# Performance work log

Measured on AMD Instinct MI355X. Metric: run time of the kernel, lower is better.

The kernel has to match this reference:

```python
import jax, jax.numpy as jnp
import numpy as np

N_NODES = 50000
N_EDGES = 800000
N_GRAPHS = 128
D_IN = 64
D_H = 64
D_OUT = 16
N_GIN_LAYERS = 4  # num_layers - 1
BN_EPS = 1e-5


def setup_inputs() -> dict:
    key = jax.random.key(0)
    ks = jax.random.split(key, 12)
    s = 0.05  # weight scale for numerical sanity
    x = jax.random.normal(ks[0], (N_NODES, D_IN), dtype=jnp.float32)
    w = jax.random.uniform(ks[1], (N_EDGES,), dtype=jnp.float32)
    src = jax.random.randint(ks[2], (N_EDGES,), 0, N_NODES, dtype=jnp.int32)
    dst = jax.random.randint(ks[3], (N_EDGES,), 0, N_NODES, dtype=jnp.int32)
    graph_ids = jnp.sort(jax.random.randint(ks[4], (N_NODES,), 0, N_GRAPHS, dtype=jnp.int32))
    eps = jnp.zeros((N_GIN_LAYERS,), dtype=jnp.float32)
    mlp_W1 = jax.random.normal(ks[5], (N_GIN_LAYERS, D_IN, D_H), dtype=jnp.float32) * s
    mlp_b1 = jnp.zeros((N_GIN_LAYERS, D_H), dtype=jnp.float32)
    mlp_bn_g = jnp.ones((N_GIN_LAYERS, D_H), dtype=jnp.float32)
    mlp_bn_b = jnp.zeros((N_GIN_LAYERS, D_H), dtype=jnp.float32)
    mlp_W2 = jax.random.normal(ks[6], (N_GIN_LAYERS, D_H, D_H), dtype=jnp.float32) * s
    mlp_b2 = jnp.zeros((N_GIN_LAYERS, D_H), dtype=jnp.float32)
    bn_g = jnp.ones((N_GIN_LAYERS, D_H), dtype=jnp.float32)
    bn_b = jnp.zeros((N_GIN_LAYERS, D_H), dtype=jnp.float32)
    pred_W = jax.random.normal(ks[7], (N_GIN_LAYERS + 1, D_H, D_OUT), dtype=jnp.float32) * s
    pred_b = jnp.zeros((N_GIN_LAYERS + 1, D_OUT), dtype=jnp.float32)
    return {"x": x, "w": w, "src": src, "dst": dst, "graph_ids": graph_ids,
            "eps": eps, "mlp_W1": mlp_W1, "mlp_b1": mlp_b1,
            "mlp_bn_g": mlp_bn_g, "mlp_bn_b": mlp_bn_b,
            "mlp_W2": mlp_W2, "mlp_b2": mlp_b2,
            "bn_g": bn_g, "bn_b": bn_b, "pred_W": pred_W, "pred_b": pred_b}


def _batchnorm(h, gamma, beta):
    # training-mode BatchNorm1d: normalize by batch mean / biased variance
    mu = jnp.mean(h, axis=0)
    var = jnp.mean((h - mu) ** 2, axis=0)
    return gamma * (h - mu) * jax.lax.rsqrt(var + BN_EPS) + beta


def reference(x, w, src, dst, graph_ids, eps, mlp_W1, mlp_b1, mlp_bn_g, mlp_bn_b,
              mlp_W2, mlp_b2, bn_g, bn_b, pred_W, pred_b):
    def pool(h):  # graph readout: sum over nodes of each graph -> [G, D]
        return jax.ops.segment_sum(h, graph_ids, num_segments=N_GRAPHS)

    h = x
    # layer-0 prediction on raw features (dropout p=0 -> identity)
    score = pool(h) @ pred_W[0] + pred_b[0]
    for l in range(N_GIN_LAYERS):
        # message: edge weight * source feature, reduce: sum over in-edges
        msg = w[:, None] * h[src]                                  # [E, D]
        h_neigh = jax.ops.segment_sum(msg, dst, num_segments=N_NODES)
        h = (1.0 + eps[l]) * h + h_neigh                           # eps self-aggregate
        # 2-layer MLP: Linear -> BN -> ReLU -> Linear
        t = _batchnorm(h @ mlp_W1[l] + mlp_b1[l], mlp_bn_g[l], mlp_bn_b[l])
        h = jax.nn.relu(t) @ mlp_W2[l] + mlp_b2[l]
        # outer BN + ReLU
        h = jax.nn.relu(_batchnorm(h, bn_g[l], bn_b[l]))
        score = score + pool(h) @ pred_W[l + 1] + pred_b[l + 1]
    return score
```

## Files before the change

kernel.cpp:

```cpp
#include <hip/hip_runtime.h>
#include <hip/hip_bf16.h>

#define N_NODES 50000
#define N_EDGES 800000
#define N_GRAPHS 128
#define NB2 391
#define BCAP 4096
#define EPB 4096
#define PART_BLOCKS ((N_EDGES + EPB - 1) / EPB)

typedef __attribute__((ext_vector_type(8))) short short8;
typedef __attribute__((ext_vector_type(4))) float f32x4;

union B16x8 { uint4 u; short8 s; };

__device__ __forceinline__ unsigned bf16rn(float f) {
    unsigned u = __float_as_uint(f);
    return (u + 0x7FFFu + ((u >> 16) & 1u)) >> 16;
}
__device__ __forceinline__ unsigned packbf2(float a, float b) {
    return bf16rn(a) | (bf16rn(b) << 16);
}
__device__ __forceinline__ float2 unpkbf2(unsigned v) {
    return make_float2(__uint_as_float(v << 16), __uint_as_float(v & 0xFFFF0000u));
}


__global__ __launch_bounds__(256) void setup_partition_kernel(
    const int* __restrict__ dst, const int* __restrict__ src, const float* __restrict__ w,
    int* __restrict__ cursor, int2* __restrict__ tmp, int E,
    const float* __restrict__ x, unsigned* __restrict__ xb,
    const float* __restrict__ W1, const float* __restrict__ W2,
    unsigned short* __restrict__ Wt, const int* __restrict__ gid,
    int* __restrict__ start, int n, int ngraphs) {
    __shared__ int lh[NB2];
    __shared__ int lbase[NB2];
    const int t = threadIdx.x;

    const int gtid = blockIdx.x * 256 + t;
    const int gsz = gridDim.x * 256;
    for (int i = gtid; i < n * 8; i += gsz) {
        float4 a = *(const float4*)(x + (size_t)i * 8);
        float4 b = *(const float4*)(x + (size_t)i * 8 + 4);
        uint4 o;
        o.x = packbf2(a.x, a.y);
        o.y = packbf2(a.z, a.w);
        o.z = packbf2(b.x, b.y);
        o.w = packbf2(b.z, b.w);
        *(uint4*)(xb + (size_t)i * 4) = o;
    }
    for (int i = gtid; i < 8 * 4096; i += gsz) {
        int mat = i >> 12, k = (i >> 6) & 63, nn = i & 63, l = mat >> 1;
        const float* Wsrc = (mat & 1) ? (W2 + l * 4096) : (W1 + l * 4096);
        Wt[(size_t)mat * 4096 + nn * 64 + k] = (unsigned short)bf16rn(Wsrc[k * 64 + nn]);
    }
    for (int i = gtid; i < n; i += gsz) {
        int g = gid[i];
        if (i == 0) {
            for (int q = 0; q <= g; ++q) start[q] = 0;
        } else {
            int p = gid[i - 1];
            if (p != g)
                for (int q = p + 1; q <= g; ++q) start[q] = i;
        }
        if (i == n - 1)
            for (int q = g + 1; q <= ngraphs; ++q) start[q] = n;
    }

    for (int i = t; i < NB2; i += 256) lh[i] = 0;
    __syncthreads();
    int base = blockIdx.x * EPB;
    int d[EPB / 256];
#pragma unroll
    for (int i = 0; i < EPB / 256; ++i) {
        int e = base + i * 256 + t;
        d[i] = (e < E) ? dst[e] : -1;
        if (d[i] >= 0) atomicAdd(&lh[d[i] >> 7], 1);
    }
    __syncthreads();
    for (int i = t; i < NB2; i += 256) {
        int v = lh[i];
        if (v) lbase[i] = atomicAdd(&cursor[i], v);
        lh[i] = 0;
    }
    __syncthreads();
#pragma unroll
    for (int i = 0; i < EPB / 256; ++i) {
        int e = base + i * 256 + t;
        if (d[i] >= 0) {
            int b = d[i] >> 7;
            int dl = d[i] & 127;
            int rank = atomicAdd(&lh[b], 1);
            tmp[(size_t)b * BCAP + lbase[b] + rank] =
                make_int2(src[e] | (dl << 16), __float_as_int(w[e]));
        }
    }
}


__global__ __launch_bounds__(256) void node_sort_kernel(const int2* __restrict__ tmp,
                                                        const int* __restrict__ ecnt,
                                                        int2* __restrict__ row_se,
                                                        unsigned* __restrict__ pack, int n) {
    __shared__ int hist[128];
    __shared__ int run[128];
    __shared__ int s[256];
    const int t = threadIdx.x;
    const int b = blockIdx.x;
    int cnt = ecnt[b];
    if (cnt > BCAP) cnt = BCAP;
    const int2* tb2 = tmp + (size_t)b * BCAP;
    const int gbase = b * BCAP;

    if (t < 128) hist[t] = 0;
    __syncthreads();
    for (int j = t; j < cnt; j += 256) atomicAdd(&hist[(tb2[j].x >> 16) & 127], 1);
    __syncthreads();
    int v = (t < 128) ? hist[t] : 0;
    s[t] = v;
    __syncthreads();
    for (int off = 1; off < 128; off <<= 1) {
        int u = (t >= off) ? s[t - off] : 0;
        __syncthreads();
        s[t] += u;
        __syncthreads();
    }
    if (t < 128) {
        int excl = s[t] - v;
        int node = b * 128 + t;
        if (node < n) row_se[node] = make_int2(gbase + excl, gbase + excl + v);
        run[t] = gbase + excl;
    }
    __syncthreads();
    for (int j = t; j < cnt; j += 256) {
        int2 p = tb2[j];
        int pos = atomicAdd(&run[(p.x >> 16) & 127], 1);
        pack[pos] = (unsigned)(p.x & 0xFFFF) | (bf16rn(__int_as_float(p.y)) << 16);
    }
}


__global__ __launch_bounds__(256) void agg_kernel(const unsigned* __restrict__ hb,
                                                  const unsigned* __restrict__ pack,
                                                  const int2* __restrict__ row_se,
                                                  const float* __restrict__ eps, int layer,
                                                  unsigned* __restrict__ outb, int n,
                                                  const float* __restrict__ stats,
                                                  const float* __restrict__ gamma,
                                                  const float* __restrict__ beta,
                                                  int transform, int agg_blocks,
                                                  const int* __restrict__ start,
                                                  const float* __restrict__ pW,
                                                  const float* __restrict__ pb,
                                                  float* __restrict__ score) {
    __shared__ float sc[64], sh[64];
    const int t = threadIdx.x;
    if (transform) {
        if (t < 64) {
            float inv_n = 1.0f / (float)n;
            float mean = stats[t] * inv_n;
            float var = stats[64 + t] * inv_n - mean * mean;
            float s = gamma[t] * rsqrtf(var + 1e-5f);
            sc[t] = s;
            sh[t] = beta[t] - mean * s;
        }
        __syncthreads();
    }

    if ((int)blockIdx.x >= agg_blocks) {
        __shared__ float red[16][68];
        __shared__ float pl[64];
        const int g = blockIdx.x - agg_blocks;
        const int r16 = t >> 4;
        const int qq = t & 15;
        const int k0 = qq << 2;
        int i0 = start[g], i1 = start[g + 1];
        float4 ps = make_float4(0.f, 0.f, 0.f, 0.f);
        for (int i = i0 + r16; i < i1; i += 16) {
            uint2 u = *(const uint2*)(hb + (size_t)i * 32 + qq * 2);
            float2 a = unpkbf2(u.x);
            float2 b = unpkbf2(u.y);
            if (transform) {
                a.x = fmaxf(fmaf(a.x, sc[k0 + 0], sh[k0 + 0]), 0.f);
                a.y = fmaxf(fmaf(a.y, sc[k0 + 1], sh[k0 + 1]), 0.f);
                b.x = fmaxf(fmaf(b.x, sc[k0 + 2], sh[k0 + 2]), 0.f);
                b.y = fmaxf(fmaf(b.y, sc[k0 + 3], sh[k0 + 3]), 0.f);
            }
            ps.x += a.x; ps.y += a.y; ps.z += b.x; ps.w += b.y;
        }
        red[r16][k0 + 0] = ps.x;
        red[r16][k0 + 1] = ps.y;
        red[r16][k0 + 2] = ps.z;
        red[r16][k0 + 3] = ps.w;
        __syncthreads();
        if (t < 64) {
            float s = 0.f;
#pragma unroll
            for (int r = 0; r < 16; ++r) s += red[r][t];
            pl[t] = s;
        }
        __syncthreads();
        if (t < 16) {
            float s = pb[t];
#pragma unroll 8
            for (int d = 0; d < 64; ++d) s += pl[d] * pW[d * 16 + t];
            score[g * 16 + t] = transform ? (score[g * 16 + t] + s) : s;
        }
        return;
    }

    int node = blockIdx.x * 4 + (t >> 6);
    if (node >= n) return;
    const int lane = t & 63;
    const int slot = lane >> 4;
    const int li = lane & 15;

    float4 sc4 = make_float4(1.f, 1.f, 1.f, 1.f);
    float4 sh4 = make_float4(0.f, 0.f, 0.f, 0.f);
    if (transform) {
        sc4 = *(const float4*)(sc + li * 4);
        sh4 = *(const float4*)(sh + li * 4);
    }
    float e1 = 1.0f + eps[layer];

    float4 acc = make_float4(0.f, 0.f, 0.f, 0.f);
    {
        uint2 su = *(const uint2*)(hb + (size_t)node * 32 + li * 2);
        if (slot == 0) {
            float2 a = unpkbf2(su.x), b = unpkbf2(su.y);
            if (transform) {
                a.x = fmaxf(fmaf(a.x, sc4.x, sh4.x), 0.f);
                a.y = fmaxf(fmaf(a.y, sc4.y, sh4.y), 0.f);
                b.x = fmaxf(fmaf(b.x, sc4.z, sh4.z), 0.f);
                b.y = fmaxf(fmaf(b.y, sc4.w, sh4.w), 0.f);
            }
            acc.x = e1 * a.x; acc.y = e1 * a.y; acc.z = e1 * b.x; acc.w = e1 * b.y;
        }
    }

    int2 se = row_se[node];
    int j0 = se.x, j1 = se.y;
    int j = j0;
    unsigned pk[4];
    if (j < j1) {
#pragma unroll
        for (int u = 0; u < 4; ++u) {
            int idx = j + slot + u * 4;
            pk[u] = pack[idx < j1 ? idx : j1 - 1];
        }
    }
    while (j < j1) {
        float wv[4];
        uint2 g[4];
#pragma unroll
        for (int u = 0; u < 4; ++u) {
            int jj = j + slot + u * 4;
            wv[u] = (jj < j1) ? __uint_as_float(pk[u] & 0xFFFF0000u) : 0.f;
        }
#pragma unroll
        for (int u = 0; u < 4; ++u)
            g[u] = *(const uint2*)(hb + (size_t)(pk[u] & 0xFFFFu) * 32 + li * 2);
        j += 16;
        if (j < j1) {
#pragma unroll
            for (int u = 0; u < 4; ++u) {
                int idx = j + slot + u * 4;
                pk[u] = pack[idx < j1 ? idx : j1 - 1];
            }
        }
#pragma unroll
        for (int u = 0; u < 4; ++u) {
            float2 a = unpkbf2(g[u].x), b = unpkbf2(g[u].y);
            if (transform) {
                a.x = fmaxf(fmaf(a.x, sc4.x, sh4.x), 0.f);
                a.y = fmaxf(fmaf(a.y, sc4.y, sh4.y), 0.f);
                b.x = fmaxf(fmaf(b.x, sc4.z, sh4.z), 0.f);
                b.y = fmaxf(fmaf(b.y, sc4.w, sh4.w), 0.f);
            }
            acc.x += wv[u] * a.x;
            acc.y += wv[u] * a.y;
            acc.z += wv[u] * b.x;
            acc.w += wv[u] * b.y;
        }
    }

    acc.x += __shfl_xor(acc.x, 16);
    acc.y += __shfl_xor(acc.y, 16);
    acc.z += __shfl_xor(acc.z, 16);
    acc.w += __shfl_xor(acc.w, 16);
    acc.x += __shfl_xor(acc.x, 32);
    acc.y += __shfl_xor(acc.y, 32);
    acc.z += __shfl_xor(acc.z, 32);
    acc.w += __shfl_xor(acc.w, 32);
    if (slot == 0) {
        uint2 o;
        o.x = packbf2(acc.x, acc.y);
        o.y = packbf2(acc.z, acc.w);
        *(uint2*)(outb + (size_t)node * 32 + li * 2) = o;
    }
}


#define GTILE 128

__global__ __launch_bounds__(256) void mfma_gemm(const unsigned short* __restrict__ A,
                                                 const unsigned short* __restrict__ Wt,
                                                 const float* __restrict__ bias,
                                                 unsigned short* __restrict__ out,
                                                 float* __restrict__ stats_out,
                                                 const float* __restrict__ stats_in,
                                                 const float* __restrict__ gamma,
                                                 const float* __restrict__ beta,
                                                 int n, int transform) {
    __shared__ float sc[64], sh[64];
    __shared__ unsigned short cstage[GTILE * 64];
    __shared__ float rsum[64 * 17];
    __shared__ float rsq[64 * 17];

    const int t = threadIdx.x;
    if (transform && t < 64) {
        float inv_n = 1.0f / (float)n;
        float mean = stats_in[t] * inv_n;
        float var = stats_in[64 + t] * inv_n - mean * mean;
        float s = gamma[t] * rsqrtf(var + 1e-5f);
        sc[t] = s;
        sh[t] = beta[t] - mean * s;
    }
    __syncthreads();

    const int wid = t >> 6;
    const int lane = t & 63;
    const int m = lane & 15;
    const int q = lane >> 4;
    const int rowbase = blockIdx.x * GTILE + wid * 32;

    B16x8 bf[4][2];
#pragma unroll
    for (int tc = 0; tc < 4; ++tc)
#pragma unroll
        for (int kc = 0; kc < 2; ++kc)
            bf[tc][kc].u = *(const uint4*)(Wt + (size_t)(tc * 16 + m) * 64 + kc * 32 + q * 8);

    B16x8 af[2][2];
#pragma unroll
    for (int tr = 0; tr < 2; ++tr) {
        int gr = rowbase + tr * 16 + m;
#pragma unroll
        for (int kc = 0; kc < 2; ++kc) {
            if (gr < n)
                af[tr][kc].u = *(const uint4*)(A + (size_t)gr * 64 + kc * 32 + q * 8);
            else
                af[tr][kc].u = make_uint4(0, 0, 0, 0);
        }
    }

    if (transform) {
        int k0base = q * 8;
#pragma unroll
        for (int tr = 0; tr < 2; ++tr)
#pragma unroll
            for (int kc = 0; kc < 2; ++kc) {
                int k0 = kc * 32 + k0base;
                float4 s0 = *(const float4*)(sc + k0);
                float4 s1 = *(const float4*)(sc + k0 + 4);
                float4 h0 = *(const float4*)(sh + k0);
                float4 h1 = *(const float4*)(sh + k0 + 4);
                uint4 uu = af[tr][kc].u;
                float2 p0 = unpkbf2(uu.x), p1 = unpkbf2(uu.y);
                float2 p2 = unpkbf2(uu.z), p3 = unpkbf2(uu.w);
                p0.x = fmaxf(fmaf(p0.x, s0.x, h0.x), 0.f);
                p0.y = fmaxf(fmaf(p0.y, s0.y, h0.y), 0.f);
                p1.x = fmaxf(fmaf(p1.x, s0.z, h0.z), 0.f);
                p1.y = fmaxf(fmaf(p1.y, s0.w, h0.w), 0.f);
                p2.x = fmaxf(fmaf(p2.x, s1.x, h1.x), 0.f);
                p2.y = fmaxf(fmaf(p2.y, s1.y, h1.y), 0.f);
                p3.x = fmaxf(fmaf(p3.x, s1.z, h1.z), 0.f);
                p3.y = fmaxf(fmaf(p3.y, s1.w, h1.w), 0.f);
                uu.x = packbf2(p0.x, p0.y);
                uu.y = packbf2(p1.x, p1.y);
                uu.z = packbf2(p2.x, p2.y);
                uu.w = packbf2(p3.x, p3.y);
                af[tr][kc].u = uu;
            }
    }

    f32x4 acc[2][4];
#pragma unroll
    for (int tr = 0; tr < 2; ++tr)
#pragma unroll
        for (int tc = 0; tc < 4; ++tc) {
            acc[tr][tc] = (f32x4){0.f, 0.f, 0.f, 0.f};
            acc[tr][tc] = __builtin_amdgcn_mfma_f32_16x16x32_bf16(af[tr][0].s, bf[tc][0].s,
                                                                  acc[tr][tc], 0, 0, 0);
            acc[tr][tc] = __builtin_amdgcn_mfma_f32_16x16x32_bf16(af[tr][1].s, bf[tc][1].s,
                                                                  acc[tr][tc], 0, 0, 0);
        }

    float bc[4];
#pragma unroll
    for (int tc = 0; tc < 4; ++tc) bc[tc] = bias[tc * 16 + m];

    float psum[4] = {0, 0, 0, 0}, psq[4] = {0, 0, 0, 0};
#pragma unroll
    for (int tr = 0; tr < 2; ++tr)
#pragma unroll
        for (int reg = 0; reg < 4; ++reg) {
            int rl = wid * 32 + tr * 16 + q * 4 + reg;
            int gr = blockIdx.x * GTILE + rl;
            int sw = ((rl >> 2) & 3) << 4;
            bool ok = gr < n;
#pragma unroll
            for (int tc = 0; tc < 4; ++tc) {
                float val = acc[tr][tc][reg] + bc[tc];
                int col = tc * 16 + m;
                cstage[rl * 64 + (col ^ sw)] = (unsigned short)bf16rn(ok ? val : 0.f);
                if (ok) {
                    psum[tc] += val;
                    psq[tc] += val * val;
                }
            }
        }

    int contrib = wid * 4 + q;
#pragma unroll
    for (int tc = 0; tc < 4; ++tc) {
        int c = tc * 16 + m;
        rsum[c * 17 + contrib] = psum[tc];
        rsq[c * 17 + contrib] = psq[tc];
    }
    __syncthreads();

#pragma unroll
    for (int rep = 0; rep < 4; ++rep) {
        int idx = rep * 256 + t;
        int rl = idx >> 3;
        int k = idx & 7;
        int gr = blockIdx.x * GTILE + rl;
        if (gr < n) {
            int klds = k ^ (((rl >> 2) & 3) << 1);
            uint4 v = *(const uint4*)(cstage + rl * 64 + klds * 8);
            *(uint4*)(out + (size_t)gr * 64 + k * 8) = v;
        }
    }

    if (t < 64) {
        float s = 0.f, qq = 0.f;
#pragma unroll
        for (int i = 0; i < 16; ++i) {
            s += rsum[t * 17 + i];
            qq += rsq[t * 17 + i];
        }
        atomicAdd(&stats_out[t], s);
        atomicAdd(&stats_out[64 + t], qq);
    }
}


__global__ __launch_bounds__(256) void pool_score_kernel(const unsigned* __restrict__ hb,
                                                         const int* __restrict__ start,
                                                         const float* __restrict__ pW,
                                                         const float* __restrict__ pb,
                                                         float* __restrict__ score,
                                                         const float* __restrict__ stats,
                                                         const float* __restrict__ gamma,
                                                         const float* __restrict__ beta,
                                                         int n, int mode) {
    __shared__ float red[16][68];
    __shared__ float sc[64], sh[64], pl[64];
    const int t = threadIdx.x;
    const int g = blockIdx.x;
    if (mode && t < 64) {
        float inv_n = 1.0f / (float)n;
        float mean = stats[t] * inv_n;
        float var = stats[64 + t] * inv_n - mean * mean;
        float s = gamma[t] * rsqrtf(var + 1e-5f);
        sc[t] = s;
        sh[t] = beta[t] - mean * s;
    }
    __syncthreads();

    const int r16 = t >> 4;
    const int qq = t & 15;
    const int k0 = qq << 2;
    int i0 = start[g], i1 = start[g + 1];
    float4 ps = make_float4(0.f, 0.f, 0.f, 0.f);
    for (int i = i0 + r16; i < i1; i += 16) {
        uint2 u = *(const uint2*)(hb + (size_t)i * 32 + qq * 2);
        float2 a = unpkbf2(u.x);
        float2 b = unpkbf2(u.y);
        if (mode) {
            a.x = fmaxf(fmaf(a.x, sc[k0 + 0], sh[k0 + 0]), 0.f);
            a.y = fmaxf(fmaf(a.y, sc[k0 + 1], sh[k0 + 1]), 0.f);
            b.x = fmaxf(fmaf(b.x, sc[k0 + 2], sh[k0 + 2]), 0.f);
            b.y = fmaxf(fmaf(b.y, sc[k0 + 3], sh[k0 + 3]), 0.f);
        }
        ps.x += a.x; ps.y += a.y; ps.z += b.x; ps.w += b.y;
    }
    red[r16][k0 + 0] = ps.x;
    red[r16][k0 + 1] = ps.y;
    red[r16][k0 + 2] = ps.z;
    red[r16][k0 + 3] = ps.w;
    __syncthreads();
    if (t < 64) {
        float s = 0.f;
#pragma unroll
        for (int r = 0; r < 16; ++r) s += red[r][t];
        pl[t] = s;
    }
    __syncthreads();
    if (t < 16) {
        float s = pb[t];
#pragma unroll 8
        for (int d = 0; d < 64; ++d) s += pl[d] * pW[d * 16 + t];
        score[g * 16 + t] = mode ? (score[g * 16 + t] + s) : s;
    }
}


extern "C" void kernel_launch(void* const* d_in, const int* in_sizes, int n_in,
                              void* d_out, int out_size, void* d_ws, size_t ws_size,
                              hipStream_t stream) {
    const float* x = (const float*)d_in[0];
    const float* w = (const float*)d_in[1];
    const int* src = (const int*)d_in[2];
    const int* dst = (const int*)d_in[3];
    const int* gid = (const int*)d_in[4];
    const float* eps = (const float*)d_in[5];
    const float* W1 = (const float*)d_in[6];
    const float* b1 = (const float*)d_in[7];
    const float* bng = (const float*)d_in[8];
    const float* bnb = (const float*)d_in[9];
    const float* W2 = (const float*)d_in[10];
    const float* b2 = (const float*)d_in[11];
    const float* og = (const float*)d_in[12];
    const float* ob = (const float*)d_in[13];
    const float* pW = (const float*)d_in[14];
    const float* pb = (const float*)d_in[15];
    float* out = (float*)d_out;

    const int N = N_NODES, E = N_EDGES, G = N_GRAPHS;

    unsigned* base = (unsigned*)d_ws;
    unsigned* xb = base;
    unsigned* HA = xb + (size_t)N * 32;
    unsigned* HB = HA + (size_t)N * 32;
    float* stats = (float*)(HB + (size_t)N * 32);
    int* cursor = (int*)(stats + 1024);
    int* start = cursor + NB2 + 1;
    int2* row_se = (int2*)(start + 132);
    unsigned short* Wt = (unsigned short*)(row_se + N + 8);
    int2* tmp = (int2*)(Wt + 8 * 4096);
    unsigned* pack = (unsigned*)(tmp + (size_t)NB2 * BCAP);

    hipMemsetAsync(stats, 0, (size_t)(1024 + NB2 + 1) * sizeof(float), stream);

    hipLaunchKernelGGL(setup_partition_kernel, dim3(PART_BLOCKS), dim3(256), 0, stream, dst, src,
                       w, cursor, tmp, E, x, xb, W1, W2, Wt, gid, start, N, G);
    hipLaunchKernelGGL(node_sort_kernel, dim3(NB2), dim3(256), 0, stream, tmp, cursor, row_se,
                       pack, N);

    const int agg_blocks = (N + 3) / 4;
    const int gemm_blocks = (N + GTILE - 1) / GTILE;
    unsigned* cur = xb;
    unsigned* P = HA;
    unsigned* Q = HB;
    for (int l = 0; l < 4; ++l) {
        const float* tr_stats = (l == 0) ? nullptr : stats + (l - 1) * 256 + 128;
        const float* tr_g = (l == 0) ? nullptr : og + (l - 1) * 64;
        const float* tr_b = (l == 0) ? nullptr : ob + (l - 1) * 64;
        hipLaunchKernelGGL(agg_kernel, dim3(agg_blocks + G), dim3(256), 0, stream, cur, pack,
                           row_se, eps, l, P, N, tr_stats, tr_g, tr_b, l == 0 ? 0 : 1,
                           agg_blocks, start, pW + (size_t)l * 1024, pb + l * 16, out);
        hipLaunchKernelGGL(mfma_gemm, dim3(gemm_blocks), dim3(256), 0, stream,
                           (const unsigned short*)P, Wt + (size_t)(l * 2) * 4096, b1 + l * 64,
                           (unsigned short*)Q, stats + l * 256, (const float*)nullptr,
                           (const float*)nullptr, (const float*)nullptr, N, 0);
        hipLaunchKernelGGL(mfma_gemm, dim3(gemm_blocks), dim3(256), 0, stream,
                           (const unsigned short*)Q, Wt + (size_t)(l * 2 + 1) * 4096, b2 + l * 64,
                           (unsigned short*)P, stats + l * 256 + 128, stats + l * 256,
                           bng + l * 64, bnb + l * 64, N, 1);
        cur = P;
        unsigned* t2 = P;
        P = Q;
        Q = t2;
    }
    hipLaunchKernelGGL(pool_score_kernel, dim3(G), dim3(256), 0, stream, cur, start,
                       pW + 4 * 1024, pb + 4 * 16, out, stats + 3 * 256 + 128, og + 3 * 64,
                       ob + 3 * 64, N, 1);
}
```

Before: 389.4 us.

## Fuse aggregation and both MLP GEMMs into one layer kernel with grid barrier

New measurement: 705.2 us. 1.81x slower.

```diff
diff --git a/kernel.cpp b/kernel.cpp
--- a/kernel.cpp
+++ b/kernel.cpp
@@ -6,8 +6,8 @@
 #define N_GRAPHS 128
 #define NB2 391
 #define BCAP 4096
-#define EPB 4096
-#define PART_BLOCKS ((N_EDGES + EPB - 1) / EPB)
+#define EPB2 2048
+#define WORKERS NB2
 
 typedef __attribute__((ext_vector_type(8))) short short8;
 typedef __attribute__((ext_vector_type(4))) float f32x4;
@@ -24,21 +24,42 @@
 __device__ __forceinline__ float2 unpkbf2(unsigned v) {
     return make_float2(__uint_as_float(v << 16), __uint_as_float(v & 0xFFFF0000u));
 }
-
-
-__global__ __launch_bounds__(256) void setup_partition_kernel(
+__device__ __forceinline__ void unpack8(uint4 g, float* f) {
+    float2 a = unpkbf2(g.x), b = unpkbf2(g.y), c = unpkbf2(g.z), d = unpkbf2(g.w);
+    f[0] = a.x; f[1] = a.y; f[2] = b.x; f[3] = b.y;
+    f[4] = c.x; f[5] = c.y; f[6] = d.x; f[7] = d.y;
+}
+
+__device__ __forceinline__ void grid_barrier(int* bar, int expected) {
+    __syncthreads();
+    if (threadIdx.x == 0) {
+        __threadfence();
+        __hip_atomic_fetch_add(bar, 1, __ATOMIC_RELEASE, __HIP_MEMORY_SCOPE_AGENT);
+        while (__hip_atomic_load(bar, __ATOMIC_ACQUIRE, __HIP_MEMORY_SCOPE_AGENT) < expected)
+            __builtin_amdgcn_s_sleep(4);
+        __threadfence();
+    }
+    __syncthreads();
+}
+
+
+__global__ __launch_bounds__(256, 2) void prep_kernel(
     const int* __restrict__ dst, const int* __restrict__ src, const float* __restrict__ w,
     int* __restrict__ cursor, int2* __restrict__ tmp, int E,
     const float* __restrict__ x, unsigned* __restrict__ xb,
     const float* __restrict__ W1, const float* __restrict__ W2,
     unsigned short* __restrict__ Wt, const int* __restrict__ gid,
-    int* __restrict__ start, int n, int ngraphs) {
+    int* __restrict__ start, int n, int ngraphs,
+    int* __restrict__ bar, int2* __restrict__ row_se, unsigned* __restrict__ pack) {
     __shared__ int lh[NB2];
     __shared__ int lbase[NB2];
+    __shared__ int hist[128];
+    __shared__ int run[128];
+    __shared__ int s[256];
     const int t = threadIdx.x;
-
     const int gtid = blockIdx.x * 256 + t;
     const int gsz = gridDim.x * 256;
+
     for (int i = gtid; i < n * 8; i += gsz) {
         float4 a = *(const float4*)(x + (size_t)i * 8);
         float4 b = *(const float4*)(x + (size_t)i * 8 + 4);
@@ -69,10 +90,10 @@
 
     for (int i = t; i < NB2; i += 256) lh[i] = 0;
     __syncthreads();
-    int base = blockIdx.x * EPB;
-    int d[EPB / 256];
-#pragma unroll
-    for (int i = 0; i < EPB / 256; ++i) {
+    int base = blockIdx.x * EPB2;
+    int d[EPB2 / 256];
+#pragma unroll
+    for (int i = 0; i < EPB2 / 256; ++i) {
         int e = base + i * 256 + t;
         d[i] = (e < E) ? dst[e] : -1;
         if (d[i] >= 0) atomicAdd(&lh[d[i] >> 7], 1);
@@ -85,29 +106,21 @@
     }
     __syncthreads();
 #pragma unroll
-    for (int i = 0; i < EPB / 256; ++i) {
+    for (int i = 0; i < EPB2 / 256; ++i) {
         int e = base + i * 256 + t;
         if (d[i] >= 0) {
-            int b = d[i] >> 7;
+            int bb = d[i] >> 7;
             int dl = d[i] & 127;
-            int rank = atomicAdd(&lh[b], 1);
-            tmp[(size_t)b * BCAP + lbase[b] + rank] =
+            int rank = atomicAdd(&lh[bb], 1);
+            tmp[(size_t)bb * BCAP + lbase[bb] + rank] =
                 make_int2(src[e] | (dl << 16), __float_as_int(w[e]));
         }
     }
-}
-
-
-__global__ __launch_bounds__(256) void node_sort_kernel(const int2* __restrict__ tmp,
-                                                        const int* __restrict__ ecnt,
-                                                        int2* __restrict__ row_se,
-                                                        unsigned* __restrict__ pack, int n) {
-    __shared__ int hist[128];
-    __shared__ int run[128];
-    __shared__ int s[256];
-    const int t = threadIdx.x;
+
+    grid_barrier(bar, (int)gridDim.x);
+
     const int b = blockIdx.x;
-    int cnt = ecnt[b];
+    int cnt = cursor[b];
     if (cnt > BCAP) cnt = BCAP;
     const int2* tb2 = tmp + (size_t)b * BCAP;
     const int gbase = b * BCAP;
@@ -120,9 +133,9 @@
     s[t] = v;
     __syncthreads();
     for (int off = 1; off < 128; off <<= 1) {
-        int u = (t >= off) ? s[t - off] : 0;
+        int u2 = (t >= off) ? s[t - off] : 0;
         __syncthreads();
-        s[t] += u;
+        s[t] += u2;
         __syncthreads();
     }
     if (t < 128) {
@@ -140,37 +153,38 @@
 }
 
 
-__global__ __launch_bounds__(256) void agg_kernel(const unsigned* __restrict__ hb,
-                                                  const unsigned* __restrict__ pack,
-                                                  const int2* __restrict__ row_se,
-                                                  const float* __restrict__ eps, int layer,
-                                                  unsigned* __restrict__ outb, int n,
-                                                  const float* __restrict__ stats,
-                                                  const float* __restrict__ gamma,
-                                                  const float* __restrict__ beta,
-                                                  int transform, int agg_blocks,
-                                                  const int* __restrict__ start,
-                                                  const float* __restrict__ pW,
-                                                  const float* __restrict__ pb,
-                                                  float* __restrict__ score) {
+__global__ __launch_bounds__(256, 2) void layer_kernel(
+    const unsigned* __restrict__ hb, const unsigned* __restrict__ pack,
+    const int2* __restrict__ row_se, const float* __restrict__ eps_arr, const int layer,
+    unsigned* __restrict__ outb, const int n,
+    const float* __restrict__ stats_prev, const float* __restrict__ g_prev,
+    const float* __restrict__ b_prev, const int transform,
+    const unsigned short* __restrict__ Wt1, const unsigned short* __restrict__ Wt2,
+    const float* __restrict__ bias1, const float* __restrict__ bias2,
+    const float* __restrict__ bn_g, const float* __restrict__ bn_b,
+    float* __restrict__ stats1, float* __restrict__ stats2, int* __restrict__ bar,
+    const int* __restrict__ start, const float* __restrict__ pW,
+    const float* __restrict__ pb, float* __restrict__ score) {
     __shared__ float sc[64], sh[64];
+    __shared__ float sc2[64], sh2[64];
+    __shared__ __align__(16) unsigned short At[128 * 64];
+    __shared__ float rsum[64 * 17], rsq[64 * 17];
+    __shared__ float red[16][68];
+    __shared__ float pl[64];
+
     const int t = threadIdx.x;
-    if (transform) {
-        if (t < 64) {
-            float inv_n = 1.0f / (float)n;
-            float mean = stats[t] * inv_n;
-            float var = stats[64 + t] * inv_n - mean * mean;
-            float s = gamma[t] * rsqrtf(var + 1e-5f);
-            sc[t] = s;
-            sh[t] = beta[t] - mean * s;
-        }
-        __syncthreads();
-    }
-
-    if ((int)blockIdx.x >= agg_blocks) {
-        __shared__ float red[16][68];
-        __shared__ float pl[64];
-        const int g = blockIdx.x - agg_blocks;
+    if (transform && t < 64) {
+        float inv_n = 1.0f / (float)n;
+        float mean = stats_prev[t] * inv_n;
+        float var = stats_prev[64 + t] * inv_n - mean * mean;
+        float s0 = g_prev[t] * rsqrtf(var + 1e-5f);
+        sc[t] = s0;
+        sh[t] = b_prev[t] - mean * s0;
+    }
+    __syncthreads();
+
+    if ((int)blockIdx.x >= WORKERS) {
+        const int g = blockIdx.x - WORKERS;
         const int r16 = t >> 4;
         const int qq = t & 15;
         const int k0 = qq << 2;
@@ -194,178 +208,264 @@
         red[r16][k0 + 3] = ps.w;
         __syncthreads();
         if (t < 64) {
-            float s = 0.f;
-#pragma unroll
-            for (int r = 0; r < 16; ++r) s += red[r][t];
-            pl[t] = s;
+            float s0 = 0.f;
+#pragma unroll
+            for (int r = 0; r < 16; ++r) s0 += red[r][t];
+            pl[t] = s0;
         }
         __syncthreads();
         if (t < 16) {
-            float s = pb[t];
+            float s0 = pb[t];
 #pragma unroll 8
-            for (int d = 0; d < 64; ++d) s += pl[d] * pW[d * 16 + t];
-            score[g * 16 + t] = transform ? (score[g * 16 + t] + s) : s;
+            for (int dd = 0; dd < 64; ++dd) s0 += pl[dd] * pW[dd * 16 + t];
+            score[g * 16 + t] = transform ? (score[g * 16 + t] + s0) : s0;
         }
         return;
     }
 
-    int node = blockIdx.x * 4 + (t >> 6);
-    if (node >= n) return;
-    const int lane = t & 63;
-    const int slot = lane >> 4;
-    const int li = lane & 15;
-
-    float4 sc4 = make_float4(1.f, 1.f, 1.f, 1.f);
-    float4 sh4 = make_float4(0.f, 0.f, 0.f, 0.f);
-    if (transform) {
-        sc4 = *(const float4*)(sc + li * 4);
-        sh4 = *(const float4*)(sh + li * 4);
-    }
-    float e1 = 1.0f + eps[layer];
-
-    float4 acc = make_float4(0.f, 0.f, 0.f, 0.f);
-    {
-        uint2 su = *(const uint2*)(hb + (size_t)node * 32 + li * 2);
-        if (slot == 0) {
-            float2 a = unpkbf2(su.x), b = unpkbf2(su.y);
-            if (transform) {
-                a.x = fmaxf(fmaf(a.x, sc4.x, sh4.x), 0.f);
-                a.y = fmaxf(fmaf(a.y, sc4.y, sh4.y), 0.f);
-                b.x = fmaxf(fmaf(b.x, sc4.z, sh4.z), 0.f);
-                b.y = fmaxf(fmaf(b.y, sc4.w, sh4.w), 0.f);
-            }
-            acc.x = e1 * a.x; acc.y = e1 * a.y; acc.z = e1 * b.x; acc.w = e1 * b.y;
-        }
-    }
-
-    int2 se = row_se[node];
-    int j0 = se.x, j1 = se.y;
-    int j = j0;
-    unsigned pk[4];
-    if (j < j1) {
-#pragma unroll
-        for (int u = 0; u < 4; ++u) {
-            int idx = j + slot + u * 4;
-            pk[u] = pack[idx < j1 ? idx : j1 - 1];
-        }
-    }
-    while (j < j1) {
-        float wv[4];
-        uint2 g[4];
-#pragma unroll
-        for (int u = 0; u < 4; ++u) {
-            int jj = j + slot + u * 4;
-            wv[u] = (jj < j1) ? __uint_as_float(pk[u] & 0xFFFF0000u) : 0.f;
-        }
-#pragma unroll
-        for (int u = 0; u < 4; ++u)
-            g[u] = *(const uint2*)(hb + (size_t)(pk[u] & 0xFFFFu) * 32 + li * 2);
-        j += 16;
-        if (j < j1) {
-#pragma unroll
-            for (int u = 0; u < 4; ++u) {
-                int idx = j + slot + u * 4;
-                pk[u] = pack[idx < j1 ? idx : j1 - 1];
-            }
-        }
-#pragma unroll
-        for (int u = 0; u < 4; ++u) {
-            float2 a = unpkbf2(g[u].x), b = unpkbf2(g[u].y);
-            if (transform) {
-                a.x = fmaxf(fmaf(a.x, sc4.x, sh4.x), 0.f);
-                a.y = fmaxf(fmaf(a.y, sc4.y, sh4.y), 0.f);
-                b.x = fmaxf(fmaf(b.x, sc4.z, sh4.z), 0.f);
-                b.y = fmaxf(fmaf(b.y, sc4.w, sh4.w), 0.f);
-            }
-            acc.x += wv[u] * a.x;
-            acc.y += wv[u] * a.y;
-            acc.z += wv[u] * b.x;
-            acc.w += wv[u] * b.y;
-        }
-    }
-
-    acc.x += __shfl_xor(acc.x, 16);
-    acc.y += __shfl_xor(acc.y, 16);
-    acc.z += __shfl_xor(acc.z, 16);
-    acc.w += __shfl_xor(acc.w, 16);
-    acc.x += __shfl_xor(acc.x, 32);
-    acc.y += __shfl_xor(acc.y, 32);
-    acc.z += __shfl_xor(acc.z, 32);
-    acc.w += __shfl_xor(acc.w, 32);
-    if (slot == 0) {
-        uint2 o;
-        o.x = packbf2(acc.x, acc.y);
-        o.y = packbf2(acc.z, acc.w);
-        *(uint2*)(outb + (size_t)node * 32 + li * 2) = o;
-    }
-}
-
-
-#define GTILE 128
-
-__global__ __launch_bounds__(256) void mfma_gemm(const unsigned short* __restrict__ A,
-                                                 const unsigned short* __restrict__ Wt,
-                                                 const float* __restrict__ bias,
-                                                 unsigned short* __restrict__ out,
-                                                 float* __restrict__ stats_out,
-                                                 const float* __restrict__ stats_in,
-                                                 const float* __restrict__ gamma,
-                                                 const float* __restrict__ beta,
-                                                 int n, int transform) {
-    __shared__ float sc[64], sh[64];
-    __shared__ unsigned short cstage[GTILE * 64];
-    __shared__ float rsum[64 * 17];
-    __shared__ float rsq[64 * 17];
-
-    const int t = threadIdx.x;
-    if (transform && t < 64) {
-        float inv_n = 1.0f / (float)n;
-        float mean = stats_in[t] * inv_n;
-        float var = stats_in[64 + t] * inv_n - mean * mean;
-        float s = gamma[t] * rsqrtf(var + 1e-5f);
-        sc[t] = s;
-        sh[t] = beta[t] - mean * s;
-    }
-    __syncthreads();
-
+    const int b = blockIdx.x;
     const int wid = t >> 6;
     const int lane = t & 63;
+    const int sl = lane >> 3;
+    const int li = lane & 7;
+
+    float scv[8], shv[8];
+#pragma unroll
+    for (int e = 0; e < 8; ++e) {
+        scv[e] = transform ? sc[li * 8 + e] : 1.f;
+        shv[e] = transform ? sh[li * 8 + e] : 0.f;
+    }
+    const float e1 = 1.0f + eps_arr[layer];
+
+    int2 se0 = make_int2(0, 0);
+    {
+        int idx = b * 128 + wid * 32 + (lane & 31);
+        if (lane < 32 && idx < n) se0 = row_se[idx];
+    }
+
+    int j0n = __shfl(se0.x, 0), j1n = __shfl(se0.y, 0);
+    unsigned pknb[4];
+    bool pknv[4];
+#pragma unroll
+    for (int u = 0; u < 4; ++u) {
+        int jj = j0n + u * 8 + sl;
+        pknv[u] = jj < j1n;
+        pknb[u] = pknv[u] ? pack[jj] : 0u;
+    }
+
+    for (int i = 0; i < 32; ++i) {
+        const int rl = wid * 32 + i;
+        const int node = b * 128 + rl;
+        const int j0 = j0n, j1 = j1n;
+        unsigned pk[4];
+        bool pv[4];
+#pragma unroll
+        for (int u = 0; u < 4; ++u) { pk[u] = pknb[u]; pv[u] = pknv[u]; }
+
+        uint4 g4[4];
+        float wv[4];
+#pragma unroll
+        for (int u = 0; u < 4; ++u) {
+            wv[u] = __uint_as_float(pk[u] & 0xFFFF0000u);
+            if (pv[u]) g4[u] = *(const uint4*)(hb + (size_t)(pk[u] & 0xFFFFu) * 32 + li * 4);
+        }
+        uint4 sv;
+        const bool selfok = (sl == 0) && (node < n);
+        if (selfok) sv = *(const uint4*)(hb + (size_t)node * 32 + li * 4);
+
+        if (i < 31) {
+            j0n = __shfl(se0.x, i + 1);
+            j1n = __shfl(se0.y, i + 1);
+#pragma unroll
+            for (int u = 0; u < 4; ++u) {
+                int jj = j0n + u * 8 + sl;
+                pknv[u] = jj < j1n;
+                pknb[u] = pknv[u] ? pack[jj] : 0u;
+            }
+        }
+
+        float acc[8];
+#pragma unroll
+        for (int e = 0; e < 8; ++e) acc[e] = 0.f;
+        if (selfok) {
+            float f[8];
+            unpack8(sv, f);
+            if (transform) {
+#pragma unroll
+                for (int e = 0; e < 8; ++e) f[e] = fmaxf(fmaf(f[e], scv[e], shv[e]), 0.f);
+            }
+#pragma unroll
+            for (int e = 0; e < 8; ++e) acc[e] = e1 * f[e];
+        }
+#pragma unroll
+        for (int u = 0; u < 4; ++u) {
+            if (pv[u]) {
+                float f[8];
+                unpack8(g4[u], f);
+                if (transform) {
+#pragma unroll
+                    for (int e = 0; e < 8; ++e) f[e] = fmaxf(fmaf(f[e], scv[e], shv[e]), 0.f);
+                }
+#pragma unroll
+                for (int e = 0; e < 8; ++e) acc[e] += wv[u] * f[e];
+            }
+        }
+        for (int j = j0 + 32; j < j1; j += 32) {
+#pragma unroll
+            for (int u = 0; u < 4; ++u) {
+                int jj = j + u * 8 + sl;
+                if (jj < j1) {
+                    unsigned p = pack[jj];
+                    float ww = __uint_as_float(p & 0xFFFF0000u);
+                    uint4 gg = *(const uint4*)(hb + (size_t)(p & 0xFFFFu) * 32 + li * 4);
+                    float f[8];
+                    unpack8(gg, f);
+                    if (transform) {
+#pragma unroll
+                        for (int e = 0; e < 8; ++e) f[e] = fmaxf(fmaf(f[e], scv[e], shv[e]), 0.f);
+                    }
+#pragma unroll
+                    for (int e = 0; e < 8; ++e) acc[e] += ww * f[e];
+                }
+            }
+        }
+#pragma unroll
+        for (int e = 0; e < 8; ++e) {
+            acc[e] += __shfl_xor(acc[e], 8);
+            acc[e] += __shfl_xor(acc[e], 16);
+            acc[e] += __shfl_xor(acc[e], 32);
+        }
+        if (sl == 0) {
+            uint4 o;
+            o.x = packbf2(acc[0], acc[1]);
+            o.y = packbf2(acc[2], acc[3]);
+            o.z = packbf2(acc[4], acc[5]);
+            o.w = packbf2(acc[6], acc[7]);
+            *(uint4*)(At + rl * 64 + ((li * 8) ^ (((rl >> 2) & 3) << 4))) = o;
+        }
+    }
+    __syncthreads();
+
     const int m = lane & 15;
     const int q = lane >> 4;
-    const int rowbase = blockIdx.x * GTILE + wid * 32;
-
-    B16x8 bf[4][2];
+
+    B16x8 bf1[4][2];
 #pragma unroll
     for (int tc = 0; tc < 4; ++tc)
 #pragma unroll
         for (int kc = 0; kc < 2; ++kc)
-            bf[tc][kc].u = *(const uint4*)(Wt + (size_t)(tc * 16 + m) * 64 + kc * 32 + q * 8);
+            bf1[tc][kc].u = *(const uint4*)(Wt1 + (size_t)(tc * 16 + m) * 64 + kc * 32 + q * 8);
 
     B16x8 af[2][2];
 #pragma unroll
     for (int tr = 0; tr < 2; ++tr) {
-        int gr = rowbase + tr * 16 + m;
-#pragma unroll
-        for (int kc = 0; kc < 2; ++kc) {
-            if (gr < n)
-                af[tr][kc].u = *(const uint4*)(A + (size_t)gr * 64 + kc * 32 + q * 8);
-            else
-                af[tr][kc].u = make_uint4(0, 0, 0, 0);
-        }
-    }
-
-    if (transform) {
+        int r = wid * 32 + tr * 16 + m;
+        int swz = ((r >> 2) & 3) << 4;
+#pragma unroll
+        for (int kc = 0; kc < 2; ++kc)
+            af[tr][kc].u = *(const uint4*)(At + r * 64 + ((kc * 32 + q * 8) ^ swz));
+    }
+
+    f32x4 acc1[2][4];
+#pragma unroll
+    for (int tr = 0; tr < 2; ++tr)
+#pragma unroll
+        for (int tc = 0; tc < 4; ++tc) {
+            acc1[tr][tc] = (f32x4){0.f, 0.f, 0.f, 0.f};
+            acc1[tr][tc] = __builtin_amdgcn_mfma_f32_16x16x32_bf16(af[tr][0].s, bf1[tc][0].s,
+                                                                   acc1[tr][tc], 0, 0, 0);
+            acc1[tr][tc] = __builtin_amdgcn_mfma_f32_16x16x32_bf16(af[tr][1].s, bf1[tc][1].s,
+                                                                   acc1[tr][tc], 0, 0, 0);
+        }
+
+    float bc[4];
+#pragma unroll
+    for (int tc = 0; tc < 4; ++tc) bc[tc] = bias1[tc * 16 + m];
+
+    __syncthreads();
+
+    float psum[4] = {0, 0, 0, 0}, psq[4] = {0, 0, 0, 0};
+#pragma unroll
+    for (int tr = 0; tr < 2; ++tr)
+#pragma unroll
+        for (int reg = 0; reg < 4; ++reg) {
+            int rl = wid * 32 + tr * 16 + q * 4 + reg;
+            int gr = b * 128 + rl;
+            int sw = ((rl >> 2) & 3) << 4;
+            bool ok = gr < n;
+#pragma unroll
+            for (int tc = 0; tc < 4; ++tc) {
+                float val = acc1[tr][tc][reg] + bc[tc];
+                int col = tc * 16 + m;
+                At[rl * 64 + (col ^ sw)] = (unsigned short)bf16rn(ok ? val : 0.f);
+                if (ok) {
+                    psum[tc] += val;
+                    psq[tc] += val * val;
+                }
+            }
+        }
+
+    int contrib = wid * 4 + q;
+#pragma unroll
+    for (int tc = 0; tc < 4; ++tc) {
+        int c = tc * 16 + m;
+        rsum[c * 17 + contrib] = psum[tc];
+        rsq[c * 17 + contrib] = psq[tc];
+    }
+    __syncthreads();
+    if (t < 64) {
+        float s0 = 0.f, qq2 = 0.f;
+#pragma unroll
+        for (int i = 0; i < 16; ++i) {
+            s0 += rsum[t * 17 + i];
+            qq2 += rsq[t * 17 + i];
+        }
+        atomicAdd(&stats1[t], s0);
+        atomicAdd(&stats1[64 + t], qq2);
+    }
+
+    grid_barrier(bar, WORKERS);
+
+    if (t < 64) {
+        float inv_n = 1.0f / (float)n;
+        float su = __hip_atomic_load(&stats1[t], __ATOMIC_RELAXED, __HIP_MEMORY_SCOPE_AGENT);
+        float sq = __hip_atomic_load(&stats1[64 + t], __ATOMIC_RELAXED, __HIP_MEMORY_SCOPE_AGENT);
+        float mean = su * inv_n;
+        float var = sq * inv_n - mean * mean;
+        float s0 = bn_g[t] * rsqrtf(var + 1e-5f);
+        sc2[t] = s0;
+        sh2[t] = bn_b[t] - mean * s0;
+    }
+    __syncthreads();
+
+    B16x8 bf2[4][2];
+#pragma unroll
+    for (int tc = 0; tc < 4; ++tc)
+#pragma unroll
+        for (int kc = 0; kc < 2; ++kc)
+            bf2[tc][kc].u = *(const uint4*)(Wt2 + (size_t)(tc * 16 + m) * 64 + kc * 32 + q * 8);
+
+    B16x8 af2[2][2];
+#pragma unroll
+    for (int tr = 0; tr < 2; ++tr) {
+        int r = wid * 32 + tr * 16 + m;
+        int swz = ((r >> 2) & 3) << 4;
+#pragma unroll
+        for (int kc = 0; kc < 2; ++kc)
+            af2[tr][kc].u = *(const uint4*)(At + r * 64 + ((kc * 32 + q * 8) ^ swz));
+    }
+    {
         int k0base = q * 8;
 #pragma unroll
         for (int tr = 0; tr < 2; ++tr)
 #pragma unroll
             for (int kc = 0; kc < 2; ++kc) {
                 int k0 = kc * 32 + k0base;
-                float4 s0 = *(const float4*)(sc + k0);
-                float4 s1 = *(const float4*)(sc + k0 + 4);
-                float4 h0 = *(const float4*)(sh + k0);
-                float4 h1 = *(const float4*)(sh + k0 + 4);
-                uint4 uu = af[tr][kc].u;
+                float4 s0 = *(const float4*)(sc2 + k0);
+                float4 s1 = *(const float4*)(sc2 + k0 + 4);
+                float4 h0 = *(const float4*)(sh2 + k0);
+                float4 h1 = *(const float4*)(sh2 + k0 + 4);
+                uint4 uu = af2[tr][kc].u;
                 float2 p0 = unpkbf2(uu.x), p1 = unpkbf2(uu.y);
                 float2 p2 = unpkbf2(uu.z), p3 = unpkbf2(uu.w);
                 p0.x = fmaxf(fmaf(p0.x, s0.x, h0.x), 0.f);
@@ -380,53 +480,53 @@
                 uu.y = packbf2(p1.x, p1.y);
                 uu.z = packbf2(p2.x, p2.y);
                 uu.w = packbf2(p3.x, p3.y);
-                af[tr][kc].u = uu;
-            }
-    }
-
-    f32x4 acc[2][4];
+                af2[tr][kc].u = uu;
+            }
+    }
+
+    f32x4 acc2[2][4];
 #pragma unroll
     for (int tr = 0; tr < 2; ++tr)
 #pragma unroll
         for (int tc = 0; tc < 4; ++tc) {
-            acc[tr][tc] = (f32x4){0.f, 0.f, 0.f, 0.f};
-            acc[tr][tc] = __builtin_amdgcn_mfma_f32_16x16x32_bf16(af[tr][0].s, bf[tc][0].s,
-                                                                  acc[tr][tc], 0, 0, 0);
-            acc[tr][tc] = __builtin_amdgcn_mfma_f32_16x16x32_bf16(af[tr][1].s, bf[tc][1].s,
-                                                                  acc[tr][tc], 0, 0, 0);
-        }
-
-    float bc[4];
-#pragma unroll
-    for (int tc = 0; tc < 4; ++tc) bc[tc] = bias[tc * 16 + m];
-
-    float psum[4] = {0, 0, 0, 0}, psq[4] = {0, 0, 0, 0};
+            acc2[tr][tc] = (f32x4){0.f, 0.f, 0.f, 0.f};
+            acc2[tr][tc] = __builtin_amdgcn_mfma_f32_16x16x32_bf16(af2[tr][0].s, bf2[tc][0].s,
+                                                                   acc2[tr][tc], 0, 0, 0);
+            acc2[tr][tc] = __builtin_amdgcn_mfma_f32_16x16x32_bf16(af2[tr][1].s, bf2[tc][1].s,
+                                                                   acc2[tr][tc], 0, 0, 0);
+        }
+
+    float bc2[4];
+#pragma unroll
+    for (int tc = 0; tc < 4; ++tc) bc2[tc] = bias2[tc * 16 + m];
+
+    __syncthreads();
+
+    float psum2[4] = {0, 0, 0, 0}, psq2[4] = {0, 0, 0, 0};
 #pragma unroll
     for (int tr = 0; tr < 2; ++tr)
 #pragma unroll
         for (int reg = 0; reg < 4; ++reg) {
             int rl = wid * 32 + tr * 16 + q * 4 + reg;
-            int gr = blockIdx.x * GTILE + rl;
+            int gr = b * 128 + rl;
             int sw = ((rl >> 2) & 3) << 4;
             bool ok = gr < n;
 #pragma unroll
             for (int tc = 0; tc < 4; ++tc) {
-                float val = acc[tr][tc][reg] + bc[tc];
+                float val = acc2[tr][tc][reg] + bc2[tc];
                 int col = tc * 16 + m;
-                cstage[rl * 64 + (col ^ sw)] = (unsigned short)bf16rn(ok ? val : 0.f);
+                At[rl * 64 + (col ^ sw)] = (unsigned short)bf16rn(ok ? val : 0.f);
                 if (ok) {
-                    psum[tc] += val;
-                    psq[tc] += val * val;
+                    psum2[tc] += val;
+                    psq2[tc] += val * val;
                 }
             }
         }
-
-    int contrib = wid * 4 + q;
 #pragma unroll
     for (int tc = 0; tc < 4; ++tc) {
         int c = tc * 16 + m;
-        rsum[c * 17 + contrib] = psum[tc];
-        rsq[c * 17 + contrib] = psq[tc];
+        rsum[c * 17 + contrib] = psum2[tc];
+        rsq[c * 17 + contrib] = psq2[tc];
     }
     __syncthreads();
 
@@ -435,23 +535,23 @@
         int idx = rep * 256 + t;
         int rl = idx >> 3;
         int k = idx & 7;
-        int gr = blockIdx.x * GTILE + rl;
+        int gr = b * 128 + rl;
         if (gr < n) {
             int klds = k ^ (((rl >> 2) & 3) << 1);
-            uint4 v = *(const uint4*)(cstage + rl * 64 + klds * 8);
-            *(uint4*)(out + (size_t)gr * 64 + k * 8) = v;
+            uint4 v = *(const uint4*)(At + rl * 64 + klds * 8);
+            *(uint4*)(outb + (size_t)gr * 32 + k * 4) = v;
         }
     }
 
     if (t < 64) {
-        float s = 0.f, qq = 0.f;
+        float s0 = 0.f, qq2 = 0.f;
 #pragma unroll
         for (int i = 0; i < 16; ++i) {
-            s += rsum[t * 17 + i];
-            qq += rsq[t * 17 + i];
-        }
-        atomicAdd(&stats_out[t], s);
-        atomicAdd(&stats_out[64 + t], qq);
+            s0 += rsum[t * 17 + i];
+            qq2 += rsq[t * 17 + i];
+        }
+        atomicAdd(&stats2[t], s0);
+        atomicAdd(&stats2[64 + t], qq2);
     }
 }
 
@@ -546,43 +646,32 @@
     unsigned* HB = HA + (size_t)N * 32;
     float* stats = (float*)(HB + (size_t)N * 32);
     int* cursor = (int*)(stats + 1024);
-    int* start = cursor + NB2 + 1;
+    int* bar = cursor + NB2 + 1;
+    int* start = bar + 8;
     int2* row_se = (int2*)(start + 132);
     unsigned short* Wt = (unsigned short*)(row_se + N + 8);
     int2* tmp = (int2*)(Wt + 8 * 4096);
     unsigned* pack = (unsigned*)(tmp + (size_t)NB2 * BCAP);
 
-    hipMemsetAsync(stats, 0, (size_t)(1024 + NB2 + 1) * sizeof(float), stream);
-
-    hipLaunchKernelGGL(setup_partition_kernel, dim3(PART_BLOCKS), dim3(256), 0, stream, dst, src,
-                       w, cursor, tmp, E, x, xb, W1, W2, Wt, gid, start, N, G);
-    hipLaunchKernelGGL(node_sort_kernel, dim3(NB2), dim3(256), 0, stream, tmp, cursor, row_se,
-                       pack, N);
-
-    const int agg_blocks = (N + 3) / 4;
-    const int gemm_blocks = (N + GTILE - 1) / GTILE;
+    hipMemsetAsync(stats, 0, (size_t)(1024 + NB2 + 1 + 8) * sizeof(float), stream);
+
+    hipLaunchKernelGGL(prep_kernel, dim3(NB2), dim3(256), 0, stream, dst, src, w, cursor,
+                       tmp, E, x, xb, W1, W2, Wt, gid, start, N, G, bar, row_se, pack);
+
+    unsigned* bufs[2] = {HA, HB};
     unsigned* cur = xb;
-    unsigned* P = HA;
-    unsigned* Q = HB;
     for (int l = 0; l < 4; ++l) {
-        const float* tr_stats = (l == 0) ? nullptr : stats + (l - 1) * 256 + 128;
-        const float* tr_g = (l == 0) ? nullptr : og + (l - 1) * 64;
-        const float* tr_b = (l == 0) ? nullptr : ob + (l - 1) * 64;
-        hipLaunchKernelGGL(agg_kernel, dim3(agg_blocks + G), dim3(256), 0, stream, cur, pack,
-                           row_se, eps, l, P, N, tr_stats, tr_g, tr_b, l == 0 ? 0 : 1,
-                           agg_blocks, start, pW + (size_t)l * 1024, pb + l * 16, out);
-        hipLaunchKernelGGL(mfma_gemm, dim3(gemm_blocks), dim3(256), 0, stream,
-                           (const unsigned short*)P, Wt + (size_t)(l * 2) * 4096, b1 + l * 64,
-                           (unsigned short*)Q, stats + l * 256, (const float*)nullptr,
-                           (const float*)nullptr, (const float*)nullptr, N, 0);
-        hipLaunchKernelGGL(mfma_gemm, dim3(gemm_blocks), dim3(256), 0, stream,
-                           (const unsigned short*)Q, Wt + (size_t)(l * 2 + 1) * 4096, b2 + l * 64,
-                           (unsigned short*)P, stats + l * 256 + 128, stats + l * 256,
-                           bng + l * 64, bnb + l * 64, N, 1);
-        cur = P;
-        unsigned* t2 = P;
-        P = Q;
-        Q = t2;
+        unsigned* nxt = bufs[l & 1];
+        const float* tp = l ? stats + (l - 1) * 256 + 128 : nullptr;
+        const float* tg = l ? og + (l - 1) * 64 : nullptr;
+        const float* tb = l ? ob + (l - 1) * 64 : nullptr;
+        hipLaunchKernelGGL(layer_kernel, dim3(WORKERS + G), dim3(256), 0, stream, cur, pack,
+                           row_se, eps, l, nxt, N, tp, tg, tb, l ? 1 : 0,
+                           Wt + (size_t)(2 * l) * 4096, Wt + (size_t)(2 * l + 1) * 4096,
+                           b1 + l * 64, b2 + l * 64, bng + l * 64, bnb + l * 64,
+                           stats + l * 256, stats + l * 256 + 128, bar + 1 + l, start,
+                           pW + (size_t)l * 1024, pb + l * 16, out);
+        cur = nxt;
     }
     hipLaunchKernelGGL(pool_score_kernel, dim3(G), dim3(256), 0, stream, cur, start,
                        pW + 4 * 1024, pb + 4 * 16, out, stats + 3 * 256 + 128, og + 3 * 64,
```
